# Kernel tuning notes

Hardware: AMD Instinct MI355X
Metric: run time of the kernel (lower is better)

The kernel has to match this reference:

```python
import jax, jax.numpy as jnp
import numpy as np

OUTPUT_SIZE = 512


def _build_schedule(n, m):
    """Static pyramid-circuit schedule of Givens/RBS gates on n wires.

    Sequential gate order (matches theta ordering): for k = 1..n-1, apply
    gates on adjacent wire pairs (i, i+1) for i = k-1 down to max(k-m, 0).
    Total gates = (2n - m - 1) * m // 2. Gates are packed into a brickwork
    schedule (timestep t = 2(k-1) - i) so each layer touches disjoint pairs
    and the whole chain runs in T = n + m - 2 parallel layers.
    Padded slots point at dummy wires (n, n+1) and are masked to identity.
    """
    layers = {}
    t_idx = 0
    for k in range(1, n):
        for i in range(k - 1, max(k - m, 0) - 1, -1):
            t = 2 * (k - 1) - i
            layers.setdefault(t, []).append((i, t_idx))
            t_idx += 1
    T = max(layers) + 1
    W = max(len(v) for v in layers.values())
    wire = np.full((T, W), n, dtype=np.int32)   # pad gates hit dummy wires (n, n+1)
    tidx = np.zeros((T, W), dtype=np.int32)
    mask = np.zeros((T, W), dtype=np.float32)
    for t, gs in layers.items():
        for j, (i, ti) in enumerate(gs):
            wire[t, j] = i
            tidx[t, j] = ti
            mask[t, j] = 1.0
    return wire, tidx, mask


def apply_orthogonal(thetas, x, output_size):
    input_size = x.shape[-1]
    n, m = max(input_size, output_size), min(input_size, output_size)
    wire, tidx, mask = _build_schedule(n, m)
    if input_size < n:
        x = jnp.pad(x, ((0, 0), (0, n - input_size)))
    state = jnp.pad(x, ((0, 0), (0, 2)))          # two dummy columns for padded gate slots
    th = thetas[jnp.asarray(tidx)]                # [T, W]
    msk = jnp.asarray(mask)
    cos = jnp.where(msk > 0, jnp.cos(th), 1.0)    # padded slots -> identity rotation
    sin = jnp.where(msk > 0, jnp.sin(th), 0.0)
    wa = jnp.asarray(wire)                        # [T, W] first wire of each pair
    wb = wa + 1

    def step(st, layer):
        c, s, a_idx, b_idx = layer
        a = st[:, a_idx]                          # [B, W]
        b = st[:, b_idx]
        st = st.at[:, a_idx].set(c * a + s * b)   # RBS rotation on each pair
        st = st.at[:, b_idx].set(c * b - s * a)
        return st, None

    state, _ = jax.lax.scan(step, state, (cos, sin, wa, wb))
    return state[:, :output_size]


def setup_inputs():
    key = jax.random.key(0)
    k1, k2 = jax.random.split(key)
    B, N = 256, 512
    n_thetas = (2 * max(N, OUTPUT_SIZE) - min(N, OUTPUT_SIZE) - 1) * min(N, OUTPUT_SIZE) // 2
    x = jax.random.normal(k1, (B, N), dtype=jnp.float32)
    thetas = jax.random.uniform(k2, (n_thetas,), dtype=jnp.float32,
                                minval=-np.pi, maxval=np.pi)
    bias = jnp.zeros((OUTPUT_SIZE,), dtype=jnp.float32)
    return {"x": x, "thetas": thetas, "bias": bias}


def reference(x, thetas, bias):
    # normalize_inputs=False path; with_bias=True
    out = apply_orthogonal(thetas, x, OUTPUT_SIZE)
    return out + bias
```

## Files before the change

kernel.cpp:

```cpp
#include <hip/hip_runtime.h>
#include <stdint.h>


#define N_WIRES 512
#define BATCH   256
#define PAIRS   510
#define PF      6
#define FINAL4  (PAIRS * 256)
#define TOTAL4  (FINAL4 + 128)
#define TOTAL2  (TOTAL4 * 2)

__global__ __launch_bounds__(256) void sincos_kernel(
    const float* __restrict__ thetas, float2* __restrict__ W2) {
  int tid = blockIdx.x * 256 + threadIdx.x;
  if (tid >= TOTAL2) return;
  int p = tid >> 9;
  int r = tid & 511;
  int q = r >> 7;
  int L = (r >> 1) & 63;
  int e = r & 1;
  int h = q >> 1;
  int t = 2 * p + h;
  int i = 8 * L + 4 * (q & 1) + 2 * e + h;
  float c = 1.0f, s = 0.0f;
  if (i <= min(t, 1020 - t)) {
    int k = ((t + i) >> 1) + 1;
    int idx = ((k * (k - 1)) >> 1) + (k - 1 - i);
    __sincosf(thetas[idx], &s, &c);
  }
  W2[tid] = make_float2(c, s);
}

__device__ __forceinline__ float dpp_shr1(float v) {
  return __int_as_float(__builtin_amdgcn_update_dpp(
      0, __float_as_int(v), 0x138, 0xF, 0xF, true));
}
__device__ __forceinline__ float dpp_shl1(float v) {
  return __int_as_float(__builtin_amdgcn_update_dpp(
      0, __float_as_int(v), 0x130, 0xF, 0xF, true));
}

__device__ __forceinline__ void gate(float& a, float& b, float c, float s) {
  float na = fmaf(c, a, s * b);
  float nb = fmaf(c, b, -(s * a));
  a = na;
  b = nb;
}

__device__ __forceinline__ void even_layer(float (&v)[8], float4 q0, float4 q1) {
  gate(v[0], v[1], q0.x, q0.y);
  gate(v[2], v[3], q0.z, q0.w);
  gate(v[4], v[5], q1.x, q1.y);
  gate(v[6], v[7], q1.z, q1.w);
}

__device__ __forceinline__ void odd_layer(float (&v)[8], float4 q2, float4 q3,
                                          int lane) {
  float cl = dpp_shr1(q3.z);
  float sl = dpp_shr1(q3.w);
  cl = (lane == 0) ? 1.0f : cl;
  float rv0 = dpp_shl1(v[0]);
  float lv7 = dpp_shr1(v[7]);
  gate(v[1], v[2], q2.x, q2.y);
  gate(v[3], v[4], q2.z, q2.w);
  gate(v[5], v[6], q3.x, q3.y);
  float nv7 = fmaf(q3.z, v[7], q3.w * rv0);
  float nv0 = fmaf(cl, v[0], -(sl * lv7));
  v[7] = nv7;
  v[0] = nv0;
}

__global__ __launch_bounds__(64, 1) void circuit_kernel(
    const float* __restrict__ x, const float* __restrict__ W,
    const float* __restrict__ bias, float* __restrict__ out) {
  const int lane = threadIdx.x;
  const int row = blockIdx.x;
  const float4* __restrict__ Wg = (const float4*)W;

  const float* xr = x + row * N_WIRES + lane * 8;
  float4 x0 = *(const float4*)(xr);
  float4 x1 = *(const float4*)(xr + 4);
  float v[8] = {x0.x, x0.y, x0.z, x0.w, x1.x, x1.y, x1.z, x1.w};

  float4 R[PF][4];
#pragma unroll
  for (int s = 0; s < PF; ++s) {
    const float4* p = Wg + s * 256 + lane;
    R[s][0] = p[0];
    R[s][1] = p[64];
    R[s][2] = p[128];
    R[s][3] = p[192];
  }

  for (int blk = 0; blk < (PAIRS / PF) - 1; ++blk) {
#pragma unroll
    for (int s = 0; s < PF; ++s) {
      asm volatile("s_waitcnt vmcnt(20)" ::: "memory");
      even_layer(v, R[s][0], R[s][1]);
      odd_layer(v, R[s][2], R[s][3], lane);
      const float4* p = Wg + (blk * PF + s + PF) * 256 + lane;
      R[s][0] = p[0];
      R[s][1] = p[64];
      R[s][2] = p[128];
      R[s][3] = p[192];
    }
  }

  asm volatile("s_waitcnt vmcnt(0)" ::: "memory");
#pragma unroll
  for (int s = 0; s < PF; ++s) {
    even_layer(v, R[s][0], R[s][1]);
    odd_layer(v, R[s][2], R[s][3], lane);
  }

  float4 f0 = Wg[FINAL4 + lane];
  float4 f1 = Wg[FINAL4 + 64 + lane];
  even_layer(v, f0, f1);

  const float* br = bias + lane * 8;
  float4 b0 = *(const float4*)(br);
  float4 b1 = *(const float4*)(br + 4);
  float4 o0 = {v[0] + b0.x, v[1] + b0.y, v[2] + b0.z, v[3] + b0.w};
  float4 o1 = {v[4] + b1.x, v[5] + b1.y, v[6] + b1.z, v[7] + b1.w};
  float* orow = out + row * N_WIRES + lane * 8;
  *(float4*)(orow) = o0;
  *(float4*)(orow + 4) = o1;
}

extern "C" void kernel_launch(void* const* d_in, const int* in_sizes, int n_in,
                              void* d_out, int out_size, void* d_ws,
                              size_t ws_size, hipStream_t stream) {
  const float* x = (const float*)d_in[0];
  const float* thetas = (const float*)d_in[1];
  const float* bias = (const float*)d_in[2];
  float* out = (float*)d_out;

  float* W = (float*)d_ws;

  sincos_kernel<<<(TOTAL2 + 255) / 256, 256, 0, stream>>>(thetas, (float2*)W);
  circuit_kernel<<<BATCH, 64, 0, stream>>>(x, W, bias, out);
}
```

Before: 133.8 us.

## Pack even-layer gates into v_pk ops, deepen prefetch, split sincos table build

The circuit kernel now holds state as float2 pairs and applies the even-layer rotations with packed v_pk_mul/v_pk_fma instructions. It folds the lane-0 boundary select into a precomputed (c-1) coefficient and raises the prefetch depth from 6 to 10 stages, with a matching vmcnt wait. The table build is split into a sincos pass over the unique thetas and a gather pass, which avoids redundant transcendental evaluation when workspace allows. The deeper prefetch costs more registers, and inline asm with op_sel flags risks sign or operand errors.

Result: faster. 114.9 us (-14.1%).

```diff
diff --git a/kernel.cpp b/kernel.cpp
--- a/kernel.cpp
+++ b/kernel.cpp
@@ -5,21 +5,46 @@
 #define N_WIRES 512
 #define BATCH   256
 #define PAIRS   510
-#define PF      6
+#define PF      10
 #define FINAL4  (PAIRS * 256)
 #define TOTAL4  (FINAL4 + 128)
 #define TOTAL2  (TOTAL4 * 2)
+#define N_THETAS 130816
 
-__global__ __launch_bounds__(256) void sincos_kernel(
+__global__ __launch_bounds__(256) void sc_kernel(
+    const float* __restrict__ thetas, float2* __restrict__ SC) {
+  int tid = blockIdx.x * 256 + threadIdx.x;
+  if (tid >= N_THETAS) return;
+  float c, s;
+  __sincosf(thetas[tid], &s, &c);
+  SC[tid] = make_float2(c, s);
+}
+
+__global__ __launch_bounds__(256) void build_kernel(
+    const float2* __restrict__ SC, float2* __restrict__ W2) {
+  int tid = blockIdx.x * 256 + threadIdx.x;
+  if (tid >= TOTAL2) return;
+  int p = tid >> 9, r = tid & 511;
+  int q = r >> 7, L = (r >> 1) & 63, e = r & 1, h = q >> 1;
+  int t = 2 * p + h;
+  int i = 8 * L + 4 * (q & 1) + 2 * e + h;
+  float c = 1.0f, s = 0.0f;
+  if (i <= min(t, 1020 - t)) {
+    int k = ((t + i) >> 1) + 1;
+    int idx = ((k * (k - 1)) >> 1) + (k - 1 - i);
+    float2 cs = SC[idx];
+    c = cs.x; s = cs.y;
+  }
+  if (q == 3 && e == 1) c -= 1.0f;
+  W2[tid] = make_float2(c, s);
+}
+
+__global__ __launch_bounds__(256) void fused_kernel(
     const float* __restrict__ thetas, float2* __restrict__ W2) {
   int tid = blockIdx.x * 256 + threadIdx.x;
   if (tid >= TOTAL2) return;
-  int p = tid >> 9;
-  int r = tid & 511;
-  int q = r >> 7;
-  int L = (r >> 1) & 63;
-  int e = r & 1;
-  int h = q >> 1;
+  int p = tid >> 9, r = tid & 511;
+  int q = r >> 7, L = (r >> 1) & 63, e = r & 1, h = q >> 1;
   int t = 2 * p + h;
   int i = 8 * L + 4 * (q & 1) + 2 * e + h;
   float c = 1.0f, s = 0.0f;
@@ -28,46 +53,61 @@
     int idx = ((k * (k - 1)) >> 1) + (k - 1 - i);
     __sincosf(thetas[idx], &s, &c);
   }
+  if (q == 3 && e == 1) c -= 1.0f;
   W2[tid] = make_float2(c, s);
 }
 
+template <int N>
+__device__ __forceinline__ void wait_vm() {
+  asm volatile("s_waitcnt vmcnt(%0)" ::"i"(N) : "memory");
+}
+
 __device__ __forceinline__ float dpp_shr1(float v) {
-  return __int_as_float(__builtin_amdgcn_update_dpp(
-      0, __float_as_int(v), 0x138, 0xF, 0xF, true));
+  return __int_as_float(
+      __builtin_amdgcn_mov_dpp(__float_as_int(v), 0x138, 0xF, 0xF, true));
 }
 __device__ __forceinline__ float dpp_shl1(float v) {
-  return __int_as_float(__builtin_amdgcn_update_dpp(
-      0, __float_as_int(v), 0x130, 0xF, 0xF, true));
+  return __int_as_float(
+      __builtin_amdgcn_mov_dpp(__float_as_int(v), 0x130, 0xF, 0xF, true));
 }
 
-__device__ __forceinline__ void gate(float& a, float& b, float c, float s) {
+__device__ __forceinline__ float2 gate_pk(float2 cs, float2 ab) {
+  float2 t, r;
+  asm("v_pk_mul_f32 %0, %1, %2 op_sel:[1,1] op_sel_hi:[1,0] neg_hi:[1,0]"
+      : "=v"(t)
+      : "v"(cs), "v"(ab));
+  asm("v_pk_fma_f32 %0, %1, %2, %3 op_sel:[0,0,0] op_sel_hi:[0,1,1]"
+      : "=v"(r)
+      : "v"(cs), "v"(ab), "v"(t));
+  return r;
+}
+
+__device__ __forceinline__ void gate_s(float& a, float& b, float c, float s) {
   float na = fmaf(c, a, s * b);
   float nb = fmaf(c, b, -(s * a));
   a = na;
   b = nb;
 }
 
-__device__ __forceinline__ void even_layer(float (&v)[8], float4 q0, float4 q1) {
-  gate(v[0], v[1], q0.x, q0.y);
-  gate(v[2], v[3], q0.z, q0.w);
-  gate(v[4], v[5], q1.x, q1.y);
-  gate(v[6], v[7], q1.z, q1.w);
-}
-
-__device__ __forceinline__ void odd_layer(float (&v)[8], float4 q2, float4 q3,
-                                          int lane) {
-  float cl = dpp_shr1(q3.z);
-  float sl = dpp_shr1(q3.w);
-  cl = (lane == 0) ? 1.0f : cl;
-  float rv0 = dpp_shl1(v[0]);
-  float lv7 = dpp_shr1(v[7]);
-  gate(v[1], v[2], q2.x, q2.y);
-  gate(v[3], v[4], q2.z, q2.w);
-  gate(v[5], v[6], q3.x, q3.y);
-  float nv7 = fmaf(q3.z, v[7], q3.w * rv0);
-  float nv0 = fmaf(cl, v[0], -(sl * lv7));
-  v[7] = nv7;
-  v[0] = nv0;
+__device__ __forceinline__ void pair_compute(float2& A, float2& B, float2& C,
+                                             float2& D, const float4& q0,
+                                             const float4& q1, const float4& q2,
+                                             const float4& q3) {
+  A = gate_pk(make_float2(q0.x, q0.y), A);
+  B = gate_pk(make_float2(q0.z, q0.w), B);
+  C = gate_pk(make_float2(q1.x, q1.y), C);
+  D = gate_pk(make_float2(q1.z, q1.w), D);
+  float cl_m1 = dpp_shr1(q3.z);
+  float sl    = dpp_shr1(q3.w);
+  float rv0 = dpp_shl1(A.x);
+  float lv7 = dpp_shr1(D.y);
+  gate_s(A.y, B.x, q2.x, q2.y);
+  gate_s(B.y, C.x, q2.z, q2.w);
+  gate_s(C.y, D.x, q3.x, q3.y);
+  float nv7 = fmaf(q3.w, rv0, fmaf(q3.z, D.y, D.y));
+  float nv0 = fmaf(-sl, lv7, fmaf(cl_m1, A.x, A.x));
+  D.y = nv7;
+  A.x = nv0;
 }
 
 __global__ __launch_bounds__(64, 1) void circuit_kernel(
@@ -80,48 +120,51 @@
   const float* xr = x + row * N_WIRES + lane * 8;
   float4 x0 = *(const float4*)(xr);
   float4 x1 = *(const float4*)(xr + 4);
-  float v[8] = {x0.x, x0.y, x0.z, x0.w, x1.x, x1.y, x1.z, x1.w};
 
   float4 R[PF][4];
+  const float4* pw = Wg + lane;
 #pragma unroll
   for (int s = 0; s < PF; ++s) {
-    const float4* p = Wg + s * 256 + lane;
-    R[s][0] = p[0];
-    R[s][1] = p[64];
-    R[s][2] = p[128];
-    R[s][3] = p[192];
+    R[s][0] = pw[0];
+    R[s][1] = pw[64];
+    R[s][2] = pw[128];
+    R[s][3] = pw[192];
+    pw += 256;
   }
+
+  float2 A = make_float2(x0.x, x0.y), B = make_float2(x0.z, x0.w);
+  float2 C = make_float2(x1.x, x1.y), D = make_float2(x1.z, x1.w);
 
   for (int blk = 0; blk < (PAIRS / PF) - 1; ++blk) {
 #pragma unroll
     for (int s = 0; s < PF; ++s) {
-      asm volatile("s_waitcnt vmcnt(20)" ::: "memory");
-      even_layer(v, R[s][0], R[s][1]);
-      odd_layer(v, R[s][2], R[s][3], lane);
-      const float4* p = Wg + (blk * PF + s + PF) * 256 + lane;
-      R[s][0] = p[0];
-      R[s][1] = p[64];
-      R[s][2] = p[128];
-      R[s][3] = p[192];
+      wait_vm<36>();
+      pair_compute(A, B, C, D, R[s][0], R[s][1], R[s][2], R[s][3]);
+      R[s][0] = pw[0];
+      R[s][1] = pw[64];
+      R[s][2] = pw[128];
+      R[s][3] = pw[192];
+      pw += 256;
     }
   }
 
-  asm volatile("s_waitcnt vmcnt(0)" ::: "memory");
+  wait_vm<0>();
 #pragma unroll
-  for (int s = 0; s < PF; ++s) {
-    even_layer(v, R[s][0], R[s][1]);
-    odd_layer(v, R[s][2], R[s][3], lane);
-  }
+  for (int s = 0; s < PF; ++s)
+    pair_compute(A, B, C, D, R[s][0], R[s][1], R[s][2], R[s][3]);
 
   float4 f0 = Wg[FINAL4 + lane];
   float4 f1 = Wg[FINAL4 + 64 + lane];
-  even_layer(v, f0, f1);
+  A = gate_pk(make_float2(f0.x, f0.y), A);
+  B = gate_pk(make_float2(f0.z, f0.w), B);
+  C = gate_pk(make_float2(f1.x, f1.y), C);
+  D = gate_pk(make_float2(f1.z, f1.w), D);
 
   const float* br = bias + lane * 8;
   float4 b0 = *(const float4*)(br);
   float4 b1 = *(const float4*)(br + 4);
-  float4 o0 = {v[0] + b0.x, v[1] + b0.y, v[2] + b0.z, v[3] + b0.w};
-  float4 o1 = {v[4] + b1.x, v[5] + b1.y, v[6] + b1.z, v[7] + b1.w};
+  float4 o0 = {A.x + b0.x, A.y + b0.y, B.x + b0.z, B.y + b0.w};
+  float4 o1 = {C.x + b1.x, C.y + b1.y, D.x + b1.z, D.y + b1.w};
   float* orow = out + row * N_WIRES + lane * 8;
   *(float4*)(orow) = o0;
   *(float4*)(orow + 4) = o1;
@@ -136,7 +179,15 @@
   float* out = (float*)d_out;
 
   float* W = (float*)d_ws;
+  size_t table_bytes = (size_t)TOTAL4 * 16;
+  size_t sc_bytes = (size_t)N_THETAS * 8;
 
-  sincos_kernel<<<(TOTAL2 + 255) / 256, 256, 0, stream>>>(thetas, (float2*)W);
+  if (ws_size >= table_bytes + sc_bytes) {
+    float2* SC = (float2*)((char*)d_ws + table_bytes);
+    sc_kernel<<<(N_THETAS + 255) / 256, 256, 0, stream>>>(thetas, SC);
+    build_kernel<<<(TOTAL2 + 255) / 256, 256, 0, stream>>>(SC, (float2*)W);
+  } else {
+    fused_kernel<<<(TOTAL2 + 255) / 256, 256, 0, stream>>>(thetas, (float2*)W);
+  }
   circuit_kernel<<<BATCH, 64, 0, stream>>>(x, W, bias, out);
 }
```
